# Kernel tuning notes

Hardware: AMD Instinct MI355X
Metric: run time of the kernel (lower is better)

Reference implementation:

```python
import jax, jax.numpy as jnp
import numpy as np

NODE_DIM = 256
EDGE_DIM = 64
TIME_DIM = 1024
HEADS = 8
HEAD_DIM = NODE_DIM // HEADS
MLP = 2
BS, N = 32, 48
BN = BS * N
E = BS * N * (N - 1)


def _lin(k, fin, fout):
    return jax.random.normal(k, (fin, fout), dtype=jnp.float32) / np.sqrt(fin)


def _edge_index():
    idx = np.arange(N)
    src, dst = np.meshgrid(idx, idx, indexing='ij')
    m = src != dst
    src, dst = src[m], dst[m]              # [N*(N-1)] per graph
    offs = (np.arange(BS) * N)[:, None]
    row = (offs + src[None, :]).reshape(-1)
    col = (offs + dst[None, :]).reshape(-1)
    return jnp.asarray(np.stack([row, col]), dtype=jnp.int32)


def setup_inputs() -> dict:
    key = jax.random.key(0)
    ks = jax.random.split(key, 32)
    d = {
        'pos': jax.random.normal(ks[0], (BN, 3), jnp.float32),
        'h': jax.random.normal(ks[1], (BN, NODE_DIM), jnp.float32),
        'edge_attr': jax.random.normal(ks[2], (E, EDGE_DIM), jnp.float32),
        'node_mask': jnp.ones((BN, 1), jnp.float32),
        'node_time_emb': jax.random.normal(ks[3], (BN, TIME_DIM), jnp.float32),
        'edge_time_emb': jax.random.normal(ks[4], (E, TIME_DIM), jnp.float32),
        'edge_index': _edge_index(),
        # edge_emb: Linear(edge_dim+1 -> edge_dim)
        'W_ee': _lin(ks[5], EDGE_DIM + 1, EDGE_DIM), 'b_ee': jnp.zeros((EDGE_DIM,)),
        # AdaLN time MLPs (SiLU -> Linear)
        'W_nt': _lin(ks[6], TIME_DIM, 6 * NODE_DIM), 'b_nt': jnp.zeros((6 * NODE_DIM,)),
        'W_et': _lin(ks[7], TIME_DIM, 6 * EDGE_DIM), 'b_et': jnp.zeros((6 * EDGE_DIM,)),
        # Trans_Layer sparse attention
        'Wq': _lin(ks[8], NODE_DIM, NODE_DIM), 'bq': jnp.zeros((NODE_DIM,)),
        'Wk': _lin(ks[9], NODE_DIM, NODE_DIM), 'bk': jnp.zeros((NODE_DIM,)),
        'Wv': _lin(ks[10], NODE_DIM, NODE_DIM), 'bv': jnp.zeros((NODE_DIM,)),
        'We0': _lin(ks[11], EDGE_DIM, NODE_DIM),
        'We1': _lin(ks[12], EDGE_DIM, NODE_DIM),
        'W_n2e': _lin(ks[13], NODE_DIM, EDGE_DIM), 'b_n2e': jnp.zeros((EDGE_DIM,)),
        # node FFN
        'W_ff1': _lin(ks[14], NODE_DIM, MLP * NODE_DIM), 'b_ff1': jnp.zeros((MLP * NODE_DIM,)),
        'W_ff2': _lin(ks[15], MLP * NODE_DIM, NODE_DIM), 'b_ff2': jnp.zeros((NODE_DIM,)),
        # edge FFN
        'W_ff3': _lin(ks[16], EDGE_DIM, MLP * EDGE_DIM), 'b_ff3': jnp.zeros((MLP * EDGE_DIM,)),
        'W_ff4': _lin(ks[17], MLP * EDGE_DIM, EDGE_DIM), 'b_ff4': jnp.zeros((EDGE_DIM,)),
        # CondEquiUpdate
        'coors_scale': jnp.full((1,), 0.01, jnp.float32),
        'W_ut': _lin(ks[18], TIME_DIM, 2 * NODE_DIM), 'b_ut': jnp.zeros((2 * NODE_DIM,)),
        'W_ui': _lin(ks[19], 2 * NODE_DIM + EDGE_DIM + 1, NODE_DIM), 'b_ui': jnp.zeros((NODE_DIM,)),
        'W_uc1': _lin(ks[20], NODE_DIM, NODE_DIM), 'b_uc1': jnp.zeros((NODE_DIM,)),
        'W_uc2': _lin(ks[21], NODE_DIM, 1),
    }
    return d


def _ln(x):  # LayerNorm, no affine, eps=1e-6
    m = x.mean(-1, keepdims=True)
    v = ((x - m) ** 2).mean(-1, keepdims=True)
    return (x - m) * jax.lax.rsqrt(v + 1e-6)


def _modulate(x, shift, scale):
    return x * (1 + scale) + shift


def _block(pos, h, edge_attr, node_mask, node_time_emb, edge_time_emb, edge_index,
           W_ee, b_ee, W_nt, b_nt, W_et, b_et, Wq, bq, Wk, bk, Wv, bv, We0, We1,
           W_n2e, b_n2e, W_ff1, b_ff1, W_ff2, b_ff2, W_ff3, b_ff3, W_ff4, b_ff4,
           coors_scale, W_ut, b_ut, W_ui, b_ui, W_uc1, b_uc1, W_uc2):
    row, col = edge_index[0], edge_index[1]  # row = source j, col = target i
    diff = pos[row] - pos[col]                              # [E,3]
    dist = jnp.sqrt(jnp.sum(diff * diff, -1, keepdims=True) + 1e-12)  # [E,1]
    ea = jnp.concatenate([dist, edge_attr], -1) @ W_ee + b_ee

    nt = jax.nn.silu(node_time_emb) @ W_nt + b_nt
    n_sh_msa, n_sc_msa, n_g_msa, n_sh_mlp, n_sc_mlp, n_g_mlp = jnp.split(nt, 6, axis=1)
    et = jax.nn.silu(edge_time_emb) @ W_et + b_et
    e_sh_msa, e_sc_msa, e_g_msa, e_sh_mlp, e_sc_mlp, e_g_mlp = jnp.split(et, 6, axis=1)

    hh = _modulate(_ln(h), n_sh_msa, n_sc_msa)
    ea = _modulate(_ln(ea), e_sh_msa, e_sc_msa)

    # sparse multi-head attention over edges (Trans_Layer)
    q = (hh @ Wq + bq).reshape(BN, HEADS, HEAD_DIM)
    k = (hh @ Wk + bk).reshape(BN, HEADS, HEAD_DIM)
    v = (hh @ Wv + bv).reshape(BN, HEADS, HEAD_DIM)
    e0 = (ea @ We0).reshape(E, HEADS, HEAD_DIM)
    e1 = (ea @ We1).reshape(E, HEADS, HEAD_DIM)
    alpha = jnp.sum(q[col] * k[row] * e0, -1) / np.sqrt(HEAD_DIM)  # [E,H]
    mx = jax.ops.segment_max(alpha, col, num_segments=BN)
    ex = jnp.exp(alpha - mx[col])
    den = jax.ops.segment_sum(ex, col, num_segments=BN)
    att = ex / (den[col] + 1e-16)
    msg = v[row] * e1 * att[:, :, None]
    h_node = jax.ops.segment_sum(msg, col, num_segments=BN).reshape(BN, NODE_DIM)

    h_edge = (h_node[row] + h_node[col]) @ W_n2e + b_n2e

    h_node = h + n_g_msa * h_node
    h_node = _modulate(_ln(h_node), n_sh_mlp, n_sc_mlp) * node_mask
    ff = jax.nn.silu(h_node @ W_ff1 + b_ff1) @ W_ff2 + b_ff2
    h_out = (h_node + n_g_mlp * ff) * node_mask

    h_e = edge_attr + e_g_msa * h_edge
    h_e = _modulate(_ln(h_e), e_sh_mlp, e_sc_mlp)
    ffe = jax.nn.silu(h_e @ W_ff3 + b_ff3) @ W_ff4 + b_ff4
    h_edge_out = h_e + e_g_mlp * ffe

    # CondEquiUpdate: equivariant coordinate update
    h_input = jnp.concatenate([h_out[row], h_out[col], h_edge_out, dist], -1)
    nrm = jnp.linalg.norm(diff, axis=-1, keepdims=True)
    cdiff = diff / jnp.clip(nrm, 1e-8) * coors_scale        # CoorsNorm(scale_init=0.01)
    t_shift, t_scale = jnp.split(jax.nn.silu(edge_time_emb) @ W_ut + b_ut, 2, axis=1)
    inv = _modulate(_ln(h_input @ W_ui + b_ui), t_shift, t_scale)
    inv = jnp.tanh(jax.nn.silu(inv @ W_uc1 + b_uc1) @ W_uc2)  # [E,1]
    trans = cdiff * inv
    pos_out = pos + jax.ops.segment_sum(trans, row, num_segments=BN)
    return h_out, h_edge_out, pos_out


def reference(pos, h, edge_attr, node_mask, node_time_emb, edge_time_emb, edge_index,
              W_ee, b_ee, W_nt, b_nt, W_et, b_et, Wq, bq, Wk, bk, Wv, bv, We0, We1,
              W_n2e, b_n2e, W_ff1, b_ff1, W_ff2, b_ff2, W_ff3, b_ff3, W_ff4, b_ff4,
              coors_scale, W_ut, b_ut, W_ui, b_ui, W_uc1, b_uc1, W_uc2):
    return _block(pos, h, edge_attr, node_mask, node_time_emb, edge_time_emb, edge_index,
                  W_ee, b_ee, W_nt, b_nt, W_et, b_et, Wq, bq, Wk, bk, Wv, bv, We0, We1,
                  W_n2e, b_n2e, W_ff1, b_ff1, W_ff2, b_ff2, W_ff3, b_ff3, W_ff4, b_ff4,
                  coors_scale, W_ut, b_ut, W_ui, b_ui, W_uc1, b_uc1, W_uc2)
```

## Files before the change

### kernel.cpp

```cpp
#include <hip/hip_runtime.h>

typedef unsigned short u16;
typedef __attribute__((ext_vector_type(4))) u16 u16x4;
typedef __attribute__((ext_vector_type(8))) u16 u16x8;
typedef __attribute__((ext_vector_type(8))) short s16x8;
typedef __attribute__((ext_vector_type(4))) float f32x4;

#define E_CNT 72192
#define BN_CNT 1536
#define EPG 2256

__device__ __forceinline__ float b2f(u16 u) {
    union { unsigned int i; float f; } x; x.i = ((unsigned int)u) << 16; return x.f;
}
__device__ __forceinline__ u16 f2b(float f) {
    union { float f; unsigned int i; } x; x.f = f;
    unsigned int r = x.i + 0x7fffu + ((x.i >> 16) & 1u);
    return (u16)(r >> 16);
}
__device__ __forceinline__ float siluf(float x) { return x / (1.f + expf(-x)); }

__device__ __forceinline__ void gll16(const void* g, void* l) {
    __builtin_amdgcn_global_load_lds(
        (const __attribute__((address_space(1))) void*)g,
        (__attribute__((address_space(3))) void*)l, 16, 0, 0);
}

__device__ __forceinline__ float wave_ln64(float x) {
    float s = x;
    #pragma unroll
    for (int off = 1; off < 64; off <<= 1) s += __shfl_xor(s, off);
    float mean = s * 0.015625f;
    float d = x - mean;
    float v2 = d * d;
    #pragma unroll
    for (int off = 1; off < 64; off <<= 1) v2 += __shfl_xor(v2, off);
    return d * rsqrtf(v2 * 0.015625f + 1e-6f);
}

__device__ __forceinline__ float block_ln256(float x) {
    __shared__ float tmp[4];
    int t = threadIdx.x;
    float s = x;
    #pragma unroll
    for (int off = 1; off < 64; off <<= 1) s += __shfl_xor(s, off);
    if ((t & 63) == 0) tmp[t >> 6] = s;
    __syncthreads();
    float mean = (tmp[0] + tmp[1] + tmp[2] + tmp[3]) * (1.f / 256.f);
    float d = x - mean;
    float v2 = d * d;
    #pragma unroll
    for (int off = 1; off < 64; off <<= 1) v2 += __shfl_xor(v2, off);
    __syncthreads();
    if ((t & 63) == 0) tmp[t >> 6] = v2;
    __syncthreads();
    float var = (tmp[0] + tmp[1] + tmp[2] + tmp[3]) * (1.f / 256.f);
    return d * rsqrtf(var + 1e-6f);
}

template<int ACT, int OUTBF>
__global__ __launch_bounds__(256) void k_gemm(
    const u16* __restrict__ A, const u16* __restrict__ Bt,
    const float* __restrict__ bias, void* __restrict__ C,
    int M, int N, int K)
{
    __shared__ u16 As[64][40];
    __shared__ u16 Bs[64][40];
    int bn0 = blockIdx.x * 64, bm0 = blockIdx.y * 64;
    int t = threadIdx.x;
    int lane = t & 63, wave = t >> 6;
    int wm = wave >> 1, wn = wave & 1;
    int lr = t >> 2, lc = (t & 3) * 8;
    f32x4 acc[2][2] = {};
    const u16* Ap = A + (size_t)(bm0 + lr) * K + lc;
    const u16* Bp = Bt + (size_t)(bn0 + lr) * K + lc;
    int fr = lane & 15, fk = (lane >> 4) * 8;
    for (int k0 = 0; k0 < K; k0 += 32) {
        *(u16x8*)&As[lr][lc] = *(const u16x8*)(Ap + k0);
        *(u16x8*)&Bs[lr][lc] = *(const u16x8*)(Bp + k0);
        __syncthreads();
        s16x8 a0 = *(const s16x8*)&As[wm * 32 + fr][fk];
        s16x8 a1 = *(const s16x8*)&As[wm * 32 + 16 + fr][fk];
        s16x8 b0 = *(const s16x8*)&Bs[wn * 32 + fr][fk];
        s16x8 b1 = *(const s16x8*)&Bs[wn * 32 + 16 + fr][fk];
        acc[0][0] = __builtin_amdgcn_mfma_f32_16x16x32_bf16(a0, b0, acc[0][0], 0, 0, 0);
        acc[0][1] = __builtin_amdgcn_mfma_f32_16x16x32_bf16(a0, b1, acc[0][1], 0, 0, 0);
        acc[1][0] = __builtin_amdgcn_mfma_f32_16x16x32_bf16(a1, b0, acc[1][0], 0, 0, 0);
        acc[1][1] = __builtin_amdgcn_mfma_f32_16x16x32_bf16(a1, b1, acc[1][1], 0, 0, 0);
        __syncthreads();
    }
    int cIn = lane & 15, r4 = (lane >> 4) * 4;
    #pragma unroll
    for (int i = 0; i < 2; i++)
    #pragma unroll
    for (int j = 0; j < 2; j++) {
        int col = bn0 + wn * 32 + j * 16 + cIn;
        float bv = bias ? bias[col] : 0.f;
        #pragma unroll
        for (int r = 0; r < 4; r++) {
            int rowg = bm0 + wm * 32 + i * 16 + r4 + r;
            float vv = acc[i][j][r] + bv;
            if (ACT == 1) vv = siluf(vv);
            if (OUTBF) ((u16*)C)[(size_t)rowg * N + col] = f2b(vv);
            else       ((float*)C)[(size_t)rowg * N + col] = vv;
        }
    }
}

__global__ __launch_bounds__(256) void k_gemm_ff2ho(
    const u16* __restrict__ A, const u16* __restrict__ Bt,
    const float* __restrict__ bias, const float* __restrict__ hmod,
    const float* __restrict__ nt, const float* __restrict__ mask,
    float* __restrict__ out, u16* __restrict__ hout_bf, int M, int N, int K)
{
    __shared__ u16 As[64][40];
    __shared__ u16 Bs[64][40];
    int bn0 = blockIdx.x * 64, bm0 = blockIdx.y * 64;
    int t = threadIdx.x;
    int lane = t & 63, wave = t >> 6;
    int wm = wave >> 1, wn = wave & 1;
    int lr = t >> 2, lc = (t & 3) * 8;
    f32x4 acc[2][2] = {};
    const u16* Ap = A + (size_t)(bm0 + lr) * K + lc;
    const u16* Bp = Bt + (size_t)(bn0 + lr) * K + lc;
    int fr = lane & 15, fk = (lane >> 4) * 8;
    for (int k0 = 0; k0 < K; k0 += 32) {
        *(u16x8*)&As[lr][lc] = *(const u16x8*)(Ap + k0);
        *(u16x8*)&Bs[lr][lc] = *(const u16x8*)(Bp + k0);
        __syncthreads();
        s16x8 a0 = *(const s16x8*)&As[wm * 32 + fr][fk];
        s16x8 a1 = *(const s16x8*)&As[wm * 32 + 16 + fr][fk];
        s16x8 b0 = *(const s16x8*)&Bs[wn * 32 + fr][fk];
        s16x8 b1 = *(const s16x8*)&Bs[wn * 32 + 16 + fr][fk];
        acc[0][0] = __builtin_amdgcn_mfma_f32_16x16x32_bf16(a0, b0, acc[0][0], 0, 0, 0);
        acc[0][1] = __builtin_amdgcn_mfma_f32_16x16x32_bf16(a0, b1, acc[0][1], 0, 0, 0);
        acc[1][0] = __builtin_amdgcn_mfma_f32_16x16x32_bf16(a1, b0, acc[1][0], 0, 0, 0);
        acc[1][1] = __builtin_amdgcn_mfma_f32_16x16x32_bf16(a1, b1, acc[1][1], 0, 0, 0);
        __syncthreads();
    }
    int cIn = lane & 15, r4 = (lane >> 4) * 4;
    #pragma unroll
    for (int i = 0; i < 2; i++)
    #pragma unroll
    for (int j = 0; j < 2; j++) {
        int col = bn0 + wn * 32 + j * 16 + cIn;
        float bv = bias[col];
        #pragma unroll
        for (int r = 0; r < 4; r++) {
            int rowg = bm0 + wm * 32 + i * 16 + r4 + r;
            float x = acc[i][j][r] + bv;
            float v = (hmod[(size_t)rowg * 256 + col]
                     + nt[(size_t)rowg * 1536 + 1280 + col] * x) * mask[rowg];
            out[(size_t)rowg * 256 + col] = v;
            hout_bf[(size_t)rowg * 256 + col] = f2b(v);
        }
    }
}

__global__ __launch_bounds__(256) void k_gemm_ff4eo(
    const u16* __restrict__ A, const u16* __restrict__ Bt,
    const float* __restrict__ bias, const float* __restrict__ hemod,
    const u16* __restrict__ etf,
    float* __restrict__ out2, u16* __restrict__ heout_bf, int M, int N, int K)
{
    __shared__ u16 As[64][40];
    __shared__ u16 Bs[64][40];
    int bn0 = blockIdx.x * 64, bm0 = blockIdx.y * 64;
    int t = threadIdx.x;
    int lane = t & 63, wave = t >> 6;
    int wm = wave >> 1, wn = wave & 1;
    int lr = t >> 2, lc = (t & 3) * 8;
    f32x4 acc[2][2] = {};
    const u16* Ap = A + (size_t)(bm0 + lr) * K + lc;
    const u16* Bp = Bt + (size_t)(bn0 + lr) * K + lc;
    int fr = lane & 15, fk = (lane >> 4) * 8;
    for (int k0 = 0; k0 < K; k0 += 32) {
        *(u16x8*)&As[lr][lc] = *(const u16x8*)(Ap + k0);
        *(u16x8*)&Bs[lr][lc] = *(const u16x8*)(Bp + k0);
        __syncthreads();
        s16x8 a0 = *(const s16x8*)&As[wm * 32 + fr][fk];
        s16x8 a1 = *(const s16x8*)&As[wm * 32 + 16 + fr][fk];
        s16x8 b0 = *(const s16x8*)&Bs[wn * 32 + fr][fk];
        s16x8 b1 = *(const s16x8*)&Bs[wn * 32 + 16 + fr][fk];
        acc[0][0] = __builtin_amdgcn_mfma_f32_16x16x32_bf16(a0, b0, acc[0][0], 0, 0, 0);
        acc[0][1] = __builtin_amdgcn_mfma_f32_16x16x32_bf16(a0, b1, acc[0][1], 0, 0, 0);
        acc[1][0] = __builtin_amdgcn_mfma_f32_16x16x32_bf16(a1, b0, acc[1][0], 0, 0, 0);
        acc[1][1] = __builtin_amdgcn_mfma_f32_16x16x32_bf16(a1, b1, acc[1][1], 0, 0, 0);
        __syncthreads();
    }
    int cIn = lane & 15, r4 = (lane >> 4) * 4;
    #pragma unroll
    for (int i = 0; i < 2; i++)
    #pragma unroll
    for (int j = 0; j < 2; j++) {
        int col = bn0 + wn * 32 + j * 16 + cIn;
        float bv = bias[col];
        #pragma unroll
        for (int r = 0; r < 4; r++) {
            int rowg = bm0 + wm * 32 + i * 16 + r4 + r;
            float x = acc[i][j][r] + bv;
            float v = hemod[(size_t)rowg * 64 + col]
                    + b2f(etf[(size_t)rowg * 896 + 320 + col]) * x;
            out2[(size_t)rowg * 64 + col] = v;
            heout_bf[(size_t)rowg * 64 + col] = f2b(v);
        }
    }
}

template<int ACT, int OUTBF>
__global__ __launch_bounds__(256) void k_gemm128(
    const u16* __restrict__ A, const u16* __restrict__ Bt,
    const float* __restrict__ bias, void* __restrict__ C,
    int M, int N, int K)
{
    __shared__ u16 As[3][128 * 32];
    __shared__ u16 Bs[3][128 * 32];
    const int t = threadIdx.x;
    const int lane = t & 63, wv = t >> 6;
    const int wm = wv >> 1, wn = wv & 1;
    const int nwg = gridDim.x * gridDim.y;
    const int orig = blockIdx.y * gridDim.x + blockIdx.x;
    const int q8 = nwg >> 3, r8 = nwg & 7;
    const int xcd = orig & 7, lin = orig >> 3;
    const int wgid = (xcd < r8 ? xcd * (q8 + 1) : r8 * (q8 + 1) + (xcd - r8) * q8) + lin;
    const int bxs = wgid % gridDim.x, bys = wgid / gridDim.x;
    const int bn0 = bxs * 128, bm0 = bys * 128;
    const int srow = t >> 2;
    const int scol = ((t & 3) ^ ((t >> 3) & 3)) * 8;
    const u16* Ap = A + (size_t)(bm0 + srow) * K + scol;
    const u16* Bp = Bt + (size_t)(bn0 + srow) * K + scol;
    const size_t rstep = (size_t)64 * K;
    const int woff = wv * 16 * 32;
    const int fr = lane & 15;
    const int fkc = (((lane >> 4) ^ ((fr >> 1) & 3)) * 8);
    f32x4 acc[4][4] = {};
    const int NT = K >> 5;

    auto STAGE = [&](int b, int ko) {
        gll16(Ap + ko, &As[b][woff]);
        gll16(Ap + ko + rstep, &As[b][woff + 64 * 32]);
        gll16(Bp + ko, &Bs[b][woff]);
        gll16(Bp + ko + rstep, &Bs[b][woff + 64 * 32]);
    };
    auto COMPUTE = [&](int b) {
        const u16* aBase = &As[b][wm * 64 * 32];
        const u16* bBase = &Bs[b][wn * 64 * 32];
        s16x8 af[4], bfr[4];
        #pragma unroll
        for (int m = 0; m < 4; m++) af[m] = *(const s16x8*)&aBase[(m * 16 + fr) * 32 + fkc];
        #pragma unroll
        for (int n = 0; n < 4; n++) bfr[n] = *(const s16x8*)&bBase[(n * 16 + fr) * 32 + fkc];
        #pragma unroll
        for (int m = 0; m < 4; m++)
        #pragma unroll
        for (int n = 0; n < 4; n++)
            acc[m][n] = __builtin_amdgcn_mfma_f32_16x16x32_bf16(af[m], bfr[n], acc[m][n], 0, 0, 0);
    };

    STAGE(0, 0);
    if (NT > 1) STAGE(1, 32);
    int cur = 0;
    for (int tt = 0; tt < NT; tt++) {
        if (tt + 2 < NT) STAGE((cur + 2) % 3, (tt + 2) * 32);
        __builtin_amdgcn_sched_barrier(0);
        int ahead = NT - 1 - tt; if (ahead > 2) ahead = 2;
        if (ahead == 2)      asm volatile("s_waitcnt vmcnt(8)" ::: "memory");
        else if (ahead == 1) asm volatile("s_waitcnt vmcnt(4)" ::: "memory");
        else                 asm volatile("s_waitcnt vmcnt(0)" ::: "memory");
        __builtin_amdgcn_sched_barrier(0);
        __builtin_amdgcn_s_barrier();
        COMPUTE(cur);
        __builtin_amdgcn_s_barrier();
        __builtin_amdgcn_sched_barrier(0);
        cur = (cur + 1) % 3;
    }

    const int cIn = lane & 15, r4 = (lane >> 4) * 4;
    #pragma unroll
    for (int n = 0; n < 4; n++) {
        int col = bn0 + wn * 64 + n * 16 + cIn;
        float bv = bias ? bias[col] : 0.f;
        #pragma unroll
        for (int m = 0; m < 4; m++) {
            #pragma unroll
            for (int r = 0; r < 4; r++) {
                int rowg = bm0 + wm * 64 + m * 16 + r4 + r;
                float vv = acc[m][n][r] + bv;
                if (ACT == 1) vv = siluf(vv);
                if (OUTBF) ((u16*)C)[(size_t)rowg * N + col] = f2b(vv);
                else       ((float*)C)[(size_t)rowg * N + col] = vv;
            }
        }
    }
}

struct GJob {
    const u16* A; const u16* Bt; const float* bias; void* C;
    int M, N, K, gx, nwg, act, outbf;
};

__global__ __launch_bounds__(256) void k_gemm128_dual(GJob ja, GJob jb)
{
    const bool first = (int)blockIdx.x < ja.nwg;
    const GJob J = first ? ja : jb;
    const int orig = first ? blockIdx.x : blockIdx.x - ja.nwg;
    __shared__ u16 As[3][128 * 32];
    __shared__ u16 Bs[3][128 * 32];
    const int t = threadIdx.x;
    const int lane = t & 63, wv = t >> 6;
    const int wm = wv >> 1, wn = wv & 1;
    const int K = J.K;
    const int q8 = J.nwg >> 3, r8 = J.nwg & 7;
    const int xcd = orig & 7, lin = orig >> 3;
    const int wgid = (xcd < r8 ? xcd * (q8 + 1) : r8 * (q8 + 1) + (xcd - r8) * q8) + lin;
    const int bxs = wgid % J.gx, bys = wgid / J.gx;
    const int bn0 = bxs * 128, bm0 = bys * 128;
    const int srow = t >> 2;
    const int scol = ((t & 3) ^ ((t >> 3) & 3)) * 8;
    const u16* Ap = J.A + (size_t)(bm0 + srow) * K + scol;
    const u16* Bp = J.Bt + (size_t)(bn0 + srow) * K + scol;
    const size_t rstep = (size_t)64 * K;
    const int woff = wv * 16 * 32;
    const int fr = lane & 15;
    const int fkc = (((lane >> 4) ^ ((fr >> 1) & 3)) * 8);
    f32x4 acc[4][4] = {};
    const int NT = K >> 5;

    auto STAGE = [&](int b, int ko) {
        gll16(Ap + ko, &As[b][woff]);
        gll16(Ap + ko + rstep, &As[b][woff + 64 * 32]);
        gll16(Bp + ko, &Bs[b][woff]);
        gll16(Bp + ko + rstep, &Bs[b][woff + 64 * 32]);
    };
    auto COMPUTE = [&](int b) {
        const u16* aBase = &As[b][wm * 64 * 32];
        const u16* bBase = &Bs[b][wn * 64 * 32];
        s16x8 af[4], bfr[4];
        #pragma unroll
        for (int m = 0; m < 4; m++) af[m] = *(const s16x8*)&aBase[(m * 16 + fr) * 32 + fkc];
        #pragma unroll
        for (int n = 0; n < 4; n++) bfr[n] = *(const s16x8*)&bBase[(n * 16 + fr) * 32 + fkc];
        #pragma unroll
        for (int m = 0; m < 4; m++)
        #pragma unroll
        for (int n = 0; n < 4; n++)
            acc[m][n] = __builtin_amdgcn_mfma_f32_16x16x32_bf16(af[m], bfr[n], acc[m][n], 0, 0, 0);
    };

    STAGE(0, 0);
    if (NT > 1) STAGE(1, 32);
    int cur = 0;
    for (int tt = 0; tt < NT; tt++) {
        if (tt + 2 < NT) STAGE((cur + 2) % 3, (tt + 2) * 32);
        __builtin_amdgcn_sched_barrier(0);
        int ahead = NT - 1 - tt; if (ahead > 2) ahead = 2;
        if (ahead == 2)      asm volatile("s_waitcnt vmcnt(8)" ::: "memory");
        else if (ahead == 1) asm volatile("s_waitcnt vmcnt(4)" ::: "memory");
        else                 asm volatile("s_waitcnt vmcnt(0)" ::: "memory");
        __builtin_amdgcn_sched_barrier(0);
        __builtin_amdgcn_s_barrier();
        COMPUTE(cur);
        __builtin_amdgcn_s_barrier();
        __builtin_amdgcn_sched_barrier(0);
        cur = (cur + 1) % 3;
    }

    const int cIn = lane & 15, r4 = (lane >> 4) * 4;
    #pragma unroll
    for (int n = 0; n < 4; n++) {
        int col = bn0 + wn * 64 + n * 16 + cIn;
        float bv = J.bias ? J.bias[col] : 0.f;
        #pragma unroll
        for (int m = 0; m < 4; m++) {
            #pragma unroll
            for (int r = 0; r < 4; r++) {
                int rowg = bm0 + wm * 64 + m * 16 + r4 + r;
                float vv = acc[m][n][r] + bv;
                if (J.act) vv = siluf(vv);
                if (J.outbf) ((u16*)J.C)[(size_t)rowg * J.N + col] = f2b(vv);
                else         ((float*)J.C)[(size_t)rowg * J.N + col] = vv;
            }
        }
    }
}

struct ConvJob { const float* W; u16* Wt; int ldw, k0, n0, K, tile_start, tiles_k; };
struct CopyJob { const float* src; float* dst; int n; };
struct BatchArgs {
    ConvJob cj[17]; CopyJob cp[5]; int conv_blocks;
    const float* sA; u16* sOA; int n4A;
    const float* sB; u16* sOB; int n4B; int silu_blocks;
};

__global__ __launch_bounds__(256) void k_prep(BatchArgs a)
{
    __shared__ float ls[64][65];
    int b = blockIdx.x;
    int t = threadIdx.x;
    if (b < a.conv_blocks) {
        int j = 0;
        #pragma unroll 1
        while (j + 1 < 17 && a.cj[j + 1].tile_start <= b) ++j;
        const ConvJob J = a.cj[j];
        int local = b - J.tile_start;
        int tk = local % J.tiles_k, tn = local / J.tiles_k;
        int k0 = tk * 64, n0 = tn * 64;
        int cn = t & 63, rk = t >> 6;
        #pragma unroll
        for (int p = 0; p < 16; p++) {
            int kk = p * 4 + rk;
            ls[kk][cn] = J.W[(size_t)(J.k0 + k0 + kk) * J.ldw + J.n0 + n0 + cn];
        }
        __syncthreads();
        int ck = t & 63, rn = t >> 6;
        #pragma unroll
        for (int p = 0; p < 16; p++) {
            int nn = p * 4 + rn;
            J.Wt[(size_t)(n0 + nn) * J.K + k0 + ck] = f2b(ls[ck][nn]);
        }
    } else if (b < a.conv_blocks + 5) {
        int c = b - a.conv_blocks;
        const CopyJob C = a.cp[c];
        for (int i = t; i < C.n; i += 256) C.dst[i] = C.src[i];
    } else {
        int sb = b - a.conv_blocks - 5;
        int total = a.n4A + a.n4B;
        int stride = a.silu_blocks * 256;
        for (int i = sb * 256 + t; i < total; i += stride) {
            const float* in; u16* out; int idx;
            if (i < a.n4A) { in = a.sA; out = a.sOA; idx = i; }
            else           { in = a.sB; out = a.sOB; idx = i - a.n4A; }
            f32x4 v = *(const f32x4*)(in + (size_t)idx * 4);
            u16x4 o;
            #pragma unroll
            for (int j = 0; j < 4; j++) o[j] = f2b(siluf(v[j]));
            *(u16x4*)(out + (size_t)idx * 4) = o;
        }
    }
}

__global__ __launch_bounds__(256) void k_edge_pre(
    const float* __restrict__ pos, const float* __restrict__ edge_attr,
    const int* __restrict__ ei, const float* __restrict__ W_ee,
    const float* __restrict__ b_ee, const float* __restrict__ coors_scale,
    const u16* __restrict__ etf,
    u16* __restrict__ ea_mod, float* __restrict__ dist, float* __restrict__ cdiff)
{
    __shared__ float Ws[65][64];
    int t = threadIdx.x;
    for (int i = t; i < 65 * 64; i += 256) Ws[i >> 6][i & 63] = W_ee[i];
    __syncthreads();
    int l = t & 63;
    float bee = b_ee[l];
    float cscale = coors_scale[0];
    for (int g = 0; g < 16; g++) {
        int e = blockIdx.x * 64 + g * 4 + (t >> 6);
        int row = ei[e], col = ei[E_CNT + e];
        float d0 = pos[row * 3 + 0] - pos[col * 3 + 0];
        float d1 = pos[row * 3 + 1] - pos[col * 3 + 1];
        float d2 = pos[row * 3 + 2] - pos[col * 3 + 2];
        float ssq = d0 * d0 + d1 * d1 + d2 * d2;
        float dst = sqrtf(ssq + 1e-12f);
        float nrm = sqrtf(ssq);
        float cs = cscale / fmaxf(nrm, 1e-8f);
        if (l == 0) {
            dist[e] = dst;
            cdiff[e * 3 + 0] = d0 * cs; cdiff[e * 3 + 1] = d1 * cs; cdiff[e * 3 + 2] = d2 * cs;
        }
        float attr = edge_attr[(size_t)e * 64 + l];
        float acc = dst * Ws[0][l];
        for (int f = 0; f < 64; f++) acc += __shfl(attr, f) * Ws[1 + f][l];
        acc += bee;
        float y = wave_ln64(acc);
        const u16* ep = etf + (size_t)e * 896;
        float m = y * (1.f + b2f(ep[64 + l])) + b2f(ep[l]);
        ea_mod[(size_t)e * 64 + l] = f2b(m);
    }
}

__global__ __launch_bounds__(256) void k_node_hh(
    const float* __restrict__ h, const float* __restrict__ nt, u16* __restrict__ hh)
{
    int n = blockIdx.x, c = threadIdx.x;
    float x = h[(size_t)n * 256 + c];
    float y = block_ln256(x);
    float m = y * (1.f + nt[(size_t)n * 1536 + 256 + c]) + nt[(size_t)n * 1536 + c];
    hh[(size_t)n * 256 + c] = f2b(m);
}

__global__ __launch_bounds__(256) void k_agg(
    const float* __restrict__ qkv, const u16* __restrict__ e01,
    float* __restrict__ hnode, u16* __restrict__ hnode_bf)
{
    int n = blockIdx.x;
    int b = n / 48, i = n % 48;
    int t = threadIdx.x;
    __shared__ float qs[8][33];
    __shared__ float att[47][8];
    __shared__ float mxs[8], dens[8];
    __shared__ int elist[47], slist[47];
    qs[t >> 5][t & 31] = qkv[(size_t)n * 768 + t];
    if (t < 47) {
        int s = t + (t >= i ? 1 : 0);
        slist[t] = s;
        elist[t] = b * EPG + s * 47 + (i < s ? i : i - 1);
    }
    __syncthreads();
    for (int idx = t; idx < 376; idx += 256) {
        int j = idx >> 3, hh = idx & 7;
        int src = b * 48 + slist[j];
        int e = elist[j];
        const float* kp = qkv + (size_t)src * 768 + 256 + hh * 32;
        const u16* ep = e01 + (size_t)e * 512 + hh * 32;
        float p = 0.f;
        #pragma unroll
        for (int d = 0; d < 32; d++) p += qs[hh][d] * kp[d] * b2f(ep[d]);
        att[j][hh] = p * 0.17677669529663687f;
    }
    __syncthreads();
    if (t < 8) {
        float m = -1e30f;
        for (int j = 0; j < 47; j++) m = fmaxf(m, att[j][t]);
        float den = 0.f;
        for (int j = 0; j < 47; j++) den += expf(att[j][t] - m);
        mxs[t] = m; dens[t] = den + 1e-16f;
    }
    __syncthreads();
    for (int idx = t; idx < 376; idx += 256) {
        int j = idx >> 3, hh = idx & 7;
        att[j][hh] = expf(att[j][hh] - mxs[hh]) / dens[hh];
    }
    __syncthreads();
    int c = t, hh = t >> 5;
    float acc = 0.f;
    for (int j = 0; j < 47; j++) {
        int src = b * 48 + slist[j];
        int e = elist[j];
        acc += att[j][hh] * qkv[(size_t)src * 768 + 512 + c] * b2f(e01[(size_t)e * 512 + 256 + c]);
    }
    hnode[(size_t)n * 256 + c] = acc;
    hnode_bf[(size_t)n * 256 + c] = f2b(acc);
}

__global__ __launch_bounds__(256) void k_mods(
    const float* __restrict__ h, const float* __restrict__ hnode_raw,
    const float* __restrict__ nt, const float* __restrict__ mask,
    float* __restrict__ hmod, u16* __restrict__ hmod_bf,
    const float* __restrict__ Q1, const float* __restrict__ b_n2e,
    const float* __restrict__ edge_attr, const int* __restrict__ ei,
    const u16* __restrict__ etf, float* __restrict__ hemod, u16* __restrict__ hemod_bf)
{
    if ((int)blockIdx.x < BN_CNT) {
        int n = blockIdx.x, c = threadIdx.x;
        float x = h[(size_t)n * 256 + c] + nt[(size_t)n * 1536 + 512 + c] * hnode_raw[(size_t)n * 256 + c];
        float y = block_ln256(x);
        float m = (y * (1.f + nt[(size_t)n * 1536 + 1024 + c]) + nt[(size_t)n * 1536 + 768 + c]) * mask[n];
        hmod[(size_t)n * 256 + c] = m;
        hmod_bf[(size_t)n * 256 + c] = f2b(m);
    } else {
        int bb = blockIdx.x - BN_CNT;
        int l = threadIdx.x & 63;
        float bn2e = b_n2e[l];
        for (int g = 0; g < 4; g++) {
            int e = bb * 16 + g * 4 + (threadIdx.x >> 6);
            int row = ei[e], col = ei[E_CNT + e];
            float hedge = Q1[(size_t)row * 64 + l] + Q1[(size_t)col * 64 + l] + bn2e;
            const u16* ep = etf + (size_t)e * 896;
            float x = edge_attr[(size_t)e * 64 + l] + b2f(ep[128 + l]) * hedge;
            float y = wave_ln64(x);
            float m = y * (1.f + b2f(ep[256 + l])) + b2f(ep[192 + l]);
            hemod[(size_t)e * 64 + l] = m;
            hemod_bf[(size_t)e * 64 + l] = f2b(m);
        }
    }
}

__global__ __launch_bounds__(256) void k_inv_pre4(
    const float* __restrict__ p12,
    const u16* __restrict__ P3, const float* __restrict__ dist,
    const float* __restrict__ W_ui, const float* __restrict__ b_ui,
    const int* __restrict__ ei, const u16* __restrict__ etf, u16* __restrict__ invmod)
{
    int e = blockIdx.x * 4 + (threadIdx.x >> 6);
    int l = threadIdx.x & 63;
    int c = l * 4;
    int row = ei[e], col = ei[E_CNT + e];
    f32x4 pa = *(const f32x4*)(p12 + (size_t)row * 512 + c);
    f32x4 pb = *(const f32x4*)(p12 + (size_t)col * 512 + 256 + c);
    u16x4 p3 = *(const u16x4*)(P3 + (size_t)e * 256 + c);
    f32x4 wui = *(const f32x4*)(W_ui + 576 * 256 + c);
    f32x4 bui = *(const f32x4*)(b_ui + c);
    float dd = dist[e];
    float x[4];
    float s = 0.f;
    #pragma unroll
    for (int j = 0; j < 4; j++) {
        x[j] = pa[j] + pb[j] + b2f(p3[j]) + dd * wui[j] + bui[j];
        s += x[j];
    }
    #pragma unroll
    for (int off = 1; off < 64; off <<= 1) s += __shfl_xor(s, off);
    float mean = s * (1.f / 256.f);
    float v2 = 0.f;
    #pragma unroll
    for (int j = 0; j < 4; j++) {
        float d = x[j] - mean;
        v2 += d * d;
    }
    #pragma unroll
    for (int off = 1; off < 64; off <<= 1) v2 += __shfl_xor(v2, off);
    float rs = rsqrtf(v2 * (1.f / 256.f) + 1e-6f);
    const u16* ep = etf + (size_t)e * 896;
    u16x4 sc = *(const u16x4*)(ep + 640 + c);
    u16x4 sh = *(const u16x4*)(ep + 384 + c);
    u16x4 o;
    #pragma unroll
    for (int j = 0; j < 4; j++) {
        float y = (x[j] - mean) * rs;
        o[j] = f2b(y * (1.f + b2f(sc[j])) + b2f(sh[j]));
    }
    *(u16x4*)(invmod + (size_t)e * 256 + c) = o;
}

__global__ __launch_bounds__(256) void k_inv(const u16* __restrict__ uc1,
                                             const float* __restrict__ W_uc2,
                                             float* __restrict__ inv)
{
    int l = threadIdx.x & 63;
    const float* w = W_uc2 + l * 4;
    float w0 = w[0], w1 = w[1], w2 = w[2], w3 = w[3];
    for (int g = 0; g < 4; g++) {
        int e = blockIdx.x * 16 + g * 4 + (threadIdx.x >> 6);
        u16x4 v = *(const u16x4*)(uc1 + (size_t)e * 256 + l * 4);
        float s = b2f(v[0]) * w0 + b2f(v[1]) * w1 + b2f(v[2]) * w2 + b2f(v[3]) * w3;
        #pragma unroll
        for (int off = 1; off < 64; off <<= 1) s += __shfl_xor(s, off);
        if (l == 0) inv[e] = tanhf(s);
    }
}

__global__ void k_pos(const float* __restrict__ pos, const float* __restrict__ cdiff,
                      const float* __restrict__ inv, float* __restrict__ out3)
{
    int n = blockIdx.x * 256 + threadIdx.x;
    if (n >= BN_CNT) return;
    int b = n / 48, s = n % 48;
    int e0 = b * EPG + s * 47;
    float a0 = 0.f, a1 = 0.f, a2 = 0.f;
    for (int j = 0; j < 47; j++) {
        float f = inv[e0 + j];
        a0 += cdiff[(size_t)(e0 + j) * 3 + 0] * f;
        a1 += cdiff[(size_t)(e0 + j) * 3 + 1] * f;
        a2 += cdiff[(size_t)(e0 + j) * 3 + 2] * f;
    }
    out3[n * 3 + 0] = pos[n * 3 + 0] + a0;
    out3[n * 3 + 1] = pos[n * 3 + 1] + a1;
    out3[n * 3 + 2] = pos[n * 3 + 2] + a2;
}

extern "C" void kernel_launch(void* const* d_in, const int* in_sizes, int n_in,
                              void* d_out, int out_size, void* d_ws, size_t ws_size,
                              hipStream_t stream)
{
    (void)in_sizes; (void)n_in; (void)out_size; (void)ws_size;
    const float* pos       = (const float*)d_in[0];
    const float* h         = (const float*)d_in[1];
    const float* edge_attr = (const float*)d_in[2];
    const float* node_mask = (const float*)d_in[3];
    const float* nte       = (const float*)d_in[4];
    const float* ete       = (const float*)d_in[5];
    const int*   ei        = (const int*)d_in[6];
    const float* W_ee = (const float*)d_in[7];  const float* b_ee = (const float*)d_in[8];
    const float* W_nt = (const float*)d_in[9];  const float* b_nt = (const float*)d_in[10];
    const float* W_et = (const float*)d_in[11]; const float* b_et = (const float*)d_in[12];
    const float* Wq  = (const float*)d_in[13];  const float* bq  = (const float*)d_in[14];
    const float* Wk  = (const float*)d_in[15];  const float* bk  = (const float*)d_in[16];
    const float* Wv  = (const float*)d_in[17];  const float* bv  = (const float*)d_in[18];
    const float* We0 = (const float*)d_in[19];  const float* We1 = (const float*)d_in[20];
    const float* W_n2e = (const float*)d_in[21]; const float* b_n2e = (const float*)d_in[22];
    const float* W_ff1 = (const float*)d_in[23]; const float* b_ff1 = (const float*)d_in[24];
    const float* W_ff2 = (const float*)d_in[25]; const float* b_ff2 = (const float*)d_in[26];
    const float* W_ff3 = (const float*)d_in[27]; const float* b_ff3 = (const float*)d_in[28];
    const float* W_ff4 = (const float*)d_in[29]; const float* b_ff4 = (const float*)d_in[30];
    const float* coors_scale = (const float*)d_in[31];
    const float* W_ut = (const float*)d_in[32]; const float* b_ut = (const float*)d_in[33];
    const float* W_ui = (const float*)d_in[34]; const float* b_ui = (const float*)d_in[35];
    const float* W_uc1 = (const float*)d_in[36]; const float* b_uc1 = (const float*)d_in[37];
    const float* W_uc2 = (const float*)d_in[38];

    const size_t E = E_CNT;
    char* ws = (char*)d_ws;
    size_t off = 0;
    auto AL = [&](size_t b) { size_t o = off; off += (b + 255) & ~(size_t)255; return o; };

    size_t o_wtcat  = AL(896 * 1024 * 2);
    size_t o_wtnt   = AL(1536 * 1024 * 2);
    size_t o_wtqkv  = AL(768 * 256 * 2);
    size_t o_wte01  = AL(512 * 64 * 2);
    size_t o_wtn2e  = AL(64 * 256 * 2);
    size_t o_wtff1  = AL(512 * 256 * 2), o_wtff2 = AL(256 * 512 * 2);
    size_t o_wtff3  = AL(128 * 64 * 2),  o_wtff4 = AL(64 * 128 * 2);
    size_t o_wtuiab = AL(512 * 256 * 2);
    size_t o_wtuic  = AL(256 * 64 * 2),  o_wtuc1 = AL(256 * 256 * 2);
    size_t o_bias896 = AL(896 * 4);
    size_t o_bias768 = AL(768 * 4);
    size_t o_reg1 = AL(E * 1024 * 2);
    size_t o_etf  = AL(E * 896 * 2);
    size_t o_ntes = AL(1536 * 1024 * 2);
    size_t o_ntf  = AL((size_t)1536 * 1536 * 4);
    size_t o_eamod = AL(E * 64 * 2);
    size_t o_dist = AL(E * 4), o_cdiff = AL(E * 12);
    size_t o_qkv  = AL(1536 * 768 * 4);
    size_t o_reg3 = AL(E * 512 * 2);
    size_t o_hnode = AL(1536 * 256 * 4), o_hnodebf = AL(1536 * 256 * 2);
    size_t o_q1 = AL(1536 * 64 * 4);
    size_t o_hh = AL(1536 * 256 * 2);
    size_t o_hmod = AL(1536 * 256 * 4), o_hmodbf = AL(1536 * 256 * 2);
    size_t o_ff1 = AL(1536 * 512 * 2);
    size_t o_houtbf = AL(1536 * 256 * 2);
    size_t o_hemod = AL(E * 64 * 4), o_hemodbf = AL(E * 64 * 2);
    size_t o_p12 = AL(1536 * 512 * 4);
    size_t o_inv = AL(E * 4);
    size_t o_etes = o_reg1;
    size_t o_p3 = o_reg1;
    size_t o_invmod = o_reg1 + E * 256 * 2;
    size_t o_uc1o = o_reg1 + E * 256 * 4;
    size_t o_e01 = o_reg3;
    size_t o_ffem = o_reg3;
    size_t o_heoutbf = o_reg3 + E * 128 * 2 + E * 64 * 4;

    #define WSU(o) ((u16*)(ws + (o)))
    #define WSF(o) ((float*)(ws + (o)))

    {
        BatchArgs a;
        int s = 0; int j = 0;
        auto add = [&](const float* W, u16* Wt, int ldw, int k0, int n0, int K, int NC) {
            a.cj[j++] = ConvJob{W, Wt, ldw, k0, n0, K, s, K / 64};
            s += (K / 64) * (NC / 64);
        };
        add(W_et, WSU(o_wtcat), 384, 0, 0, 1024, 384);
        add(W_ut, WSU(o_wtcat) + (size_t)384 * 1024, 512, 0, 0, 1024, 512);
        add(W_nt, WSU(o_wtnt), 1536, 0, 0, 1024, 1536);
        add(Wq, WSU(o_wtqkv), 256, 0, 0, 256, 256);
        add(Wk, WSU(o_wtqkv) + (size_t)256 * 256, 256, 0, 0, 256, 256);
        add(Wv, WSU(o_wtqkv) + (size_t)512 * 256, 256, 0, 0, 256, 256);
        add(We0, WSU(o_wte01), 256, 0, 0, 64, 256);
        add(We1, WSU(o_wte01) + (size_t)256 * 64, 256, 0, 0, 64, 256);
        add(W_n2e, WSU(o_wtn2e), 64, 0, 0, 256, 64);
        add(W_ff1, WSU(o_wtff1), 512, 0, 0, 256, 512);
        add(W_ff2, WSU(o_wtff2), 256, 0, 0, 512, 256);
        add(W_ff3, WSU(o_wtff3), 128, 0, 0, 64, 128);
        add(W_ff4, WSU(o_wtff4), 64, 0, 0, 128, 64);
        add(W_ui, WSU(o_wtuiab), 256, 0, 0, 256, 256);
        add(W_ui, WSU(o_wtuiab) + (size_t)256 * 256, 256, 256, 0, 256, 256);
        add(W_ui, WSU(o_wtuic), 256, 512, 0, 64, 256);
        add(W_uc1, WSU(o_wtuc1), 256, 0, 0, 256, 256);
        a.conv_blocks = s;
        a.cp[0] = CopyJob{b_et, WSF(o_bias896), 384};
        a.cp[1] = CopyJob{b_ut, WSF(o_bias896) + 384, 512};
        a.cp[2] = CopyJob{bq, WSF(o_bias768), 256};
        a.cp[3] = CopyJob{bk, WSF(o_bias768) + 256, 256};
        a.cp[4] = CopyJob{bv, WSF(o_bias768) + 512, 256};
        a.sA = ete; a.sOA = WSU(o_etes); a.n4A = (int)(E * 1024 / 4);
        a.sB = nte; a.sOB = WSU(o_ntes); a.n4B = 1536 * 1024 / 4;
        a.silu_blocks = 2048;
        k_prep<<<s + 5 + 2048, 256, 0, stream>>>(a);
    }

    {
        GJob ja{WSU(o_etes), WSU(o_wtcat), WSF(o_bias896), WSU(o_etf),
                E_CNT, 896, 1024, 7, 3948, 0, 1};
        GJob jb{WSU(o_ntes), WSU(o_wtnt), b_nt, WSF(o_ntf),
                1536, 1536, 1024, 12, 144, 0, 0};
        k_gemm128_dual<<<3948 + 144, 256, 0, stream>>>(ja, jb);
    }

    k_edge_pre<<<1128, 256, 0, stream>>>(pos, edge_attr, ei, W_ee, b_ee, coors_scale,
                                         WSU(o_etf), WSU(o_eamod), WSF(o_dist), WSF(o_cdiff));
    k_node_hh<<<1536, 256, 0, stream>>>(h, WSF(o_ntf), WSU(o_hh));

    {
        GJob ja{WSU(o_eamod), WSU(o_wte01), nullptr, WSU(o_e01),
                E_CNT, 512, 64, 4, 2256, 0, 1};
        GJob jb{WSU(o_hh), WSU(o_wtqkv), WSF(o_bias768), WSF(o_qkv),
                1536, 768, 256, 6, 72, 0, 0};
        k_gemm128_dual<<<2256 + 72, 256, 0, stream>>>(ja, jb);
    }
    k_agg<<<1536, 256, 0, stream>>>(WSF(o_qkv), WSU(o_e01), WSF(o_hnode), WSU(o_hnodebf));

    k_gemm<0, 0><<<dim3(1, 24), 256, 0, stream>>>(WSU(o_hnodebf), WSU(o_wtn2e), nullptr, WSF(o_q1), 1536, 64, 256);

    k_mods<<<BN_CNT + 4512, 256, 0, stream>>>(
        h, WSF(o_hnode), WSF(o_ntf), node_mask, WSF(o_hmod), WSU(o_hmodbf),
        WSF(o_q1), b_n2e, edge_attr, ei, WSU(o_etf), WSF(o_hemod), WSU(o_hemodbf));

    {
        GJob ja{WSU(o_hemodbf), WSU(o_wtff3), b_ff3, WSU(o_ffem),
                E_CNT, 128, 64, 1, 564, 1, 1};
        GJob jb{WSU(o_hmodbf), WSU(o_wtff1), b_ff1, WSU(o_ff1),
                1536, 512, 256, 4, 48, 1, 1};
        k_gemm128_dual<<<564 + 48, 256, 0, stream>>>(ja, jb);
    }

    k_gemm_ff2ho<<<dim3(4, 24), 256, 0, stream>>>(WSU(o_ff1), WSU(o_wtff2), b_ff2,
                                                  WSF(o_hmod), WSF(o_ntf), node_mask,
                                                  (float*)d_out, WSU(o_houtbf), 1536, 256, 512);
    k_gemm_ff4eo<<<dim3(1, 1128), 256, 0, stream>>>(WSU(o_ffem), WSU(o_wtff4), b_ff4,
                                                    WSF(o_hemod), WSU(o_etf),
                                                    (float*)d_out + 393216, WSU(o_heoutbf), E_CNT, 64, 128);

    {
        GJob ja{WSU(o_heoutbf), WSU(o_wtuic), nullptr, WSU(o_p3),
                E_CNT, 256, 64, 2, 1128, 0, 1};
        GJob jb{WSU(o_houtbf), WSU(o_wtuiab), nullptr, WSF(o_p12),
                1536, 512, 256, 4, 48, 0, 0};
        k_gemm128_dual<<<1128 + 48, 256, 0, stream>>>(ja, jb);
    }
    k_inv_pre4<<<18048, 256, 0, stream>>>(WSF(o_p12), WSU(o_p3), WSF(o_dist),
                                          W_ui, b_ui, ei, WSU(o_etf), WSU(o_invmod));
    k_gemm128<1, 1><<<dim3(2, 564), 256, 0, stream>>>(WSU(o_invmod), WSU(o_wtuc1), b_uc1, WSU(o_uc1o), E_CNT, 256, 256);
    k_inv<<<4512, 256, 0, stream>>>(WSU(o_uc1o), W_uc2, WSF(o_inv));
    k_pos<<<6, 256, 0, stream>>>(pos, WSF(o_cdiff), WSF(o_inv), (float*)d_out + 393216 + E_CNT * 64);

    #undef WSU
    #undef WSF
}
```

Before: 675.2 us.

## Merge independent kernels into combined launches and fuse n2e projection into aggregation

Combines the edge-pre and node-LN kernels into one launch with block-range dispatch, and merges the two FF-output GEMM epilogue kernels into one launch the same way. It also folds the small hnode×W_n2e GEMM into the attention aggregation kernel, which now computes q1 per node with a shared-memory dot product. This removes three kernel launches and their serialization gaps. The cost is a scalar per-block reduction in place of a small MFMA GEMM, plus extra shared memory in k_agg.

```diff
diff --git a/kernel.cpp b/kernel.cpp
--- a/kernel.cpp
+++ b/kernel.cpp
@@ -107,15 +107,27 @@
     }
 }
 
-__global__ __launch_bounds__(256) void k_gemm_ff2ho(
-    const u16* __restrict__ A, const u16* __restrict__ Bt,
-    const float* __restrict__ bias, const float* __restrict__ hmod,
+__global__ __launch_bounds__(256) void k_ffout(
+    const u16* __restrict__ A1, const u16* __restrict__ Bt1,
+    const float* __restrict__ bias1, const float* __restrict__ hmod,
     const float* __restrict__ nt, const float* __restrict__ mask,
-    float* __restrict__ out, u16* __restrict__ hout_bf, int M, int N, int K)
+    float* __restrict__ out1, u16* __restrict__ hout_bf,
+    const u16* __restrict__ A2, const u16* __restrict__ Bt2,
+    const float* __restrict__ bias2, const float* __restrict__ hemod,
+    const u16* __restrict__ etf,
+    float* __restrict__ out2, u16* __restrict__ heout_bf)
 {
     __shared__ u16 As[64][40];
     __shared__ u16 Bs[64][40];
-    int bn0 = blockIdx.x * 64, bm0 = blockIdx.y * 64;
+    const bool first = (int)blockIdx.x < 96;
+    const u16* A = first ? A1 : A2;
+    const u16* Bt = first ? Bt1 : Bt2;
+    const float* bias = first ? bias1 : bias2;
+    const int N = first ? 256 : 64;
+    const int K = first ? 512 : 128;
+    int bn0, bm0;
+    if (first) { bn0 = ((int)blockIdx.x % 4) * 64; bm0 = ((int)blockIdx.x / 4) * 64; }
+    else       { bn0 = 0; bm0 = ((int)blockIdx.x - 96) * 64; }
     int t = threadIdx.x;
     int lane = t & 63, wave = t >> 6;
     int wm = wave >> 1, wn = wave & 1;
@@ -149,60 +161,17 @@
         for (int r = 0; r < 4; r++) {
             int rowg = bm0 + wm * 32 + i * 16 + r4 + r;
             float x = acc[i][j][r] + bv;
-            float v = (hmod[(size_t)rowg * 256 + col]
-                     + nt[(size_t)rowg * 1536 + 1280 + col] * x) * mask[rowg];
-            out[(size_t)rowg * 256 + col] = v;
-            hout_bf[(size_t)rowg * 256 + col] = f2b(v);
-        }
-    }
-}
-
-__global__ __launch_bounds__(256) void k_gemm_ff4eo(
-    const u16* __restrict__ A, const u16* __restrict__ Bt,
-    const float* __restrict__ bias, const float* __restrict__ hemod,
-    const u16* __restrict__ etf,
-    float* __restrict__ out2, u16* __restrict__ heout_bf, int M, int N, int K)
-{
-    __shared__ u16 As[64][40];
-    __shared__ u16 Bs[64][40];
-    int bn0 = blockIdx.x * 64, bm0 = blockIdx.y * 64;
-    int t = threadIdx.x;
-    int lane = t & 63, wave = t >> 6;
-    int wm = wave >> 1, wn = wave & 1;
-    int lr = t >> 2, lc = (t & 3) * 8;
-    f32x4 acc[2][2] = {};
-    const u16* Ap = A + (size_t)(bm0 + lr) * K + lc;
-    const u16* Bp = Bt + (size_t)(bn0 + lr) * K + lc;
-    int fr = lane & 15, fk = (lane >> 4) * 8;
-    for (int k0 = 0; k0 < K; k0 += 32) {
-        *(u16x8*)&As[lr][lc] = *(const u16x8*)(Ap + k0);
-        *(u16x8*)&Bs[lr][lc] = *(const u16x8*)(Bp + k0);
-        __syncthreads();
-        s16x8 a0 = *(const s16x8*)&As[wm * 32 + fr][fk];
-        s16x8 a1 = *(const s16x8*)&As[wm * 32 + 16 + fr][fk];
-        s16x8 b0 = *(const s16x8*)&Bs[wn * 32 + fr][fk];
-        s16x8 b1 = *(const s16x8*)&Bs[wn * 32 + 16 + fr][fk];
-        acc[0][0] = __builtin_amdgcn_mfma_f32_16x16x32_bf16(a0, b0, acc[0][0], 0, 0, 0);
-        acc[0][1] = __builtin_amdgcn_mfma_f32_16x16x32_bf16(a0, b1, acc[0][1], 0, 0, 0);
-        acc[1][0] = __builtin_amdgcn_mfma_f32_16x16x32_bf16(a1, b0, acc[1][0], 0, 0, 0);
-        acc[1][1] = __builtin_amdgcn_mfma_f32_16x16x32_bf16(a1, b1, acc[1][1], 0, 0, 0);
-        __syncthreads();
-    }
-    int cIn = lane & 15, r4 = (lane >> 4) * 4;
-    #pragma unroll
-    for (int i = 0; i < 2; i++)
-    #pragma unroll
-    for (int j = 0; j < 2; j++) {
-        int col = bn0 + wn * 32 + j * 16 + cIn;
-        float bv = bias[col];
-        #pragma unroll
-        for (int r = 0; r < 4; r++) {
-            int rowg = bm0 + wm * 32 + i * 16 + r4 + r;
-            float x = acc[i][j][r] + bv;
-            float v = hemod[(size_t)rowg * 64 + col]
-                    + b2f(etf[(size_t)rowg * 896 + 320 + col]) * x;
-            out2[(size_t)rowg * 64 + col] = v;
-            heout_bf[(size_t)rowg * 64 + col] = f2b(v);
+            if (first) {
+                float v = (hmod[(size_t)rowg * 256 + col]
+                         + nt[(size_t)rowg * 1536 + 1280 + col] * x) * mask[rowg];
+                out1[(size_t)rowg * 256 + col] = v;
+                hout_bf[(size_t)rowg * 256 + col] = f2b(v);
+            } else {
+                float v = hemod[(size_t)rowg * 64 + col]
+                        + b2f(etf[(size_t)rowg * 896 + 320 + col]) * x;
+                out2[(size_t)rowg * 64 + col] = v;
+                heout_bf[(size_t)rowg * 64 + col] = f2b(v);
+            }
         }
     }
 }
@@ -439,58 +408,58 @@
     }
 }
 
-__global__ __launch_bounds__(256) void k_edge_pre(
+__global__ __launch_bounds__(256) void k_pre2(
     const float* __restrict__ pos, const float* __restrict__ edge_attr,
     const int* __restrict__ ei, const float* __restrict__ W_ee,
     const float* __restrict__ b_ee, const float* __restrict__ coors_scale,
     const u16* __restrict__ etf,
-    u16* __restrict__ ea_mod, float* __restrict__ dist, float* __restrict__ cdiff)
-{
-    __shared__ float Ws[65][64];
+    u16* __restrict__ ea_mod, float* __restrict__ dist, float* __restrict__ cdiff,
+    const float* __restrict__ h, const float* __restrict__ nt, u16* __restrict__ hh)
+{
     int t = threadIdx.x;
-    for (int i = t; i < 65 * 64; i += 256) Ws[i >> 6][i & 63] = W_ee[i];
-    __syncthreads();
-    int l = t & 63;
-    float bee = b_ee[l];
-    float cscale = coors_scale[0];
-    for (int g = 0; g < 16; g++) {
-        int e = blockIdx.x * 64 + g * 4 + (t >> 6);
-        int row = ei[e], col = ei[E_CNT + e];
-        float d0 = pos[row * 3 + 0] - pos[col * 3 + 0];
-        float d1 = pos[row * 3 + 1] - pos[col * 3 + 1];
-        float d2 = pos[row * 3 + 2] - pos[col * 3 + 2];
-        float ssq = d0 * d0 + d1 * d1 + d2 * d2;
-        float dst = sqrtf(ssq + 1e-12f);
-        float nrm = sqrtf(ssq);
-        float cs = cscale / fmaxf(nrm, 1e-8f);
-        if (l == 0) {
-            dist[e] = dst;
-            cdiff[e * 3 + 0] = d0 * cs; cdiff[e * 3 + 1] = d1 * cs; cdiff[e * 3 + 2] = d2 * cs;
+    if ((int)blockIdx.x < 1128) {
+        __shared__ float Ws[65][64];
+        for (int i = t; i < 65 * 64; i += 256) Ws[i >> 6][i & 63] = W_ee[i];
+        __syncthreads();
+        int l = t & 63;
+        float bee = b_ee[l];
+        float cscale = coors_scale[0];
+        for (int g = 0; g < 16; g++) {
+            int e = blockIdx.x * 64 + g * 4 + (t >> 6);
+            int row = ei[e], col = ei[E_CNT + e];
+            float d0 = pos[row * 3 + 0] - pos[col * 3 + 0];
+            float d1 = pos[row * 3 + 1] - pos[col * 3 + 1];
+            float d2 = pos[row * 3 + 2] - pos[col * 3 + 2];
+            float ssq = d0 * d0 + d1 * d1 + d2 * d2;
+            float dst = sqrtf(ssq + 1e-12f);
+            float nrm = sqrtf(ssq);
+            float cs = cscale / fmaxf(nrm, 1e-8f);
+            if (l == 0) {
+                dist[e] = dst;
+                cdiff[e * 3 + 0] = d0 * cs; cdiff[e * 3 + 1] = d1 * cs; cdiff[e * 3 + 2] = d2 * cs;
+            }
+            float attr = edge_attr[(size_t)e * 64 + l];
+            float acc = dst * Ws[0][l];
+            for (int f = 0; f < 64; f++) acc += __shfl(attr, f) * Ws[1 + f][l];
+            acc += bee;
+            float y = wave_ln64(acc);
+            const u16* ep = etf + (size_t)e * 896;
+            float m = y * (1.f + b2f(ep[64 + l])) + b2f(ep[l]);
+            ea_mod[(size_t)e * 64 + l] = f2b(m);
         }
-        float attr = edge_attr[(size_t)e * 64 + l];
-        float acc = dst * Ws[0][l];
-        for (int f = 0; f < 64; f++) acc += __shfl(attr, f) * Ws[1 + f][l];
-        acc += bee;
-        float y = wave_ln64(acc);
-        const u16* ep = etf + (size_t)e * 896;
-        float m = y * (1.f + b2f(ep[64 + l])) + b2f(ep[l]);
-        ea_mod[(size_t)e * 64 + l] = f2b(m);
-    }
-}
-
-__global__ __launch_bounds__(256) void k_node_hh(
-    const float* __restrict__ h, const float* __restrict__ nt, u16* __restrict__ hh)
-{
-    int n = blockIdx.x, c = threadIdx.x;
-    float x = h[(size_t)n * 256 + c];
-    float y = block_ln256(x);
-    float m = y * (1.f + nt[(size_t)n * 1536 + 256 + c]) + nt[(size_t)n * 1536 + c];
-    hh[(size_t)n * 256 + c] = f2b(m);
+    } else {
+        int n = blockIdx.x - 1128, c = t;
+        float x = h[(size_t)n * 256 + c];
+        float y = block_ln256(x);
+        float m = y * (1.f + nt[(size_t)n * 1536 + 256 + c]) + nt[(size_t)n * 1536 + c];
+        hh[(size_t)n * 256 + c] = f2b(m);
+    }
 }
 
 __global__ __launch_bounds__(256) void k_agg(
     const float* __restrict__ qkv, const u16* __restrict__ e01,
-    float* __restrict__ hnode, u16* __restrict__ hnode_bf)
+    const u16* __restrict__ wtn2e,
+    float* __restrict__ hnode, u16* __restrict__ hnode_bf, float* __restrict__ q1)
 {
     int n = blockIdx.x;
     int b = n / 48, i = n % 48;
@@ -499,6 +468,8 @@
     __shared__ float att[47][8];
     __shared__ float mxs[8], dens[8];
     __shared__ int elist[47], slist[47];
+    __shared__ float hs[256];
+    __shared__ float q1s[4][64];
     qs[t >> 5][t & 31] = qkv[(size_t)n * 768 + t];
     if (t < 47) {
         int s = t + (t >= i ? 1 : 0);
@@ -538,8 +509,20 @@
         int e = elist[j];
         acc += att[j][hh] * qkv[(size_t)src * 768 + 512 + c] * b2f(e01[(size_t)e * 512 + 256 + c]);
     }
+    u16 abf = f2b(acc);
     hnode[(size_t)n * 256 + c] = acc;
-    hnode_bf[(size_t)n * 256 + c] = f2b(acc);
+    hnode_bf[(size_t)n * 256 + c] = abf;
+    hs[c] = b2f(abf);
+    __syncthreads();
+    int jq = t & 63, p = t >> 6;
+    const u16* wrow = wtn2e + (size_t)jq * 256 + p * 64;
+    const float* hrow = hs + p * 64;
+    float part = 0.f;
+    #pragma unroll
+    for (int cc = 0; cc < 64; cc++) part += hrow[cc] * b2f(wrow[cc]);
+    q1s[p][jq] = part;
+    __syncthreads();
+    if (t < 64) q1[(size_t)n * 64 + t] = q1s[0][t] + q1s[1][t] + q1s[2][t] + q1s[3][t];
 }
 
 __global__ __launch_bounds__(256) void k_mods(
@@ -776,9 +759,10 @@
         k_gemm128_dual<<<3948 + 144, 256, 0, stream>>>(ja, jb);
     }
 
-    k_edge_pre<<<1128, 256, 0, stream>>>(pos, edge_attr, ei, W_ee, b_ee, coors_scale,
-                                         WSU(o_etf), WSU(o_eamod), WSF(o_dist), WSF(o_cdiff));
-    k_node_hh<<<1536, 256, 0, stream>>>(h, WSF(o_ntf), WSU(o_hh));
+    k_pre2<<<1128 + 1536, 256, 0, stream>>>(
+        pos, edge_attr, ei, W_ee, b_ee, coors_scale,
+        WSU(o_etf), WSU(o_eamod), WSF(o_dist), WSF(o_cdiff),
+        h, WSF(o_ntf), WSU(o_hh));
 
     {
         GJob ja{WSU(o_eamod), WSU(o_wte01), nullptr, WSU(o_e01),
@@ -787,9 +771,8 @@
                 1536, 768, 256, 6, 72, 0, 0};
         k_gemm128_dual<<<2256 + 72, 256, 0, stream>>>(ja, jb);
     }
-    k_agg<<<1536, 256, 0, stream>>>(WSF(o_qkv), WSU(o_e01), WSF(o_hnode), WSU(o_hnodebf));
-
-    k_gemm<0, 0><<<dim3(1, 24), 256, 0, stream>>>(WSU(o_hnodebf), WSU(o_wtn2e), nullptr, WSF(o_q1), 1536, 64, 256);
+    k_agg<<<1536, 256, 0, stream>>>(WSF(o_qkv), WSU(o_e01), WSU(o_wtn2e),
+                                    WSF(o_hnode), WSU(o_hnodebf), WSF(o_q1));
 
     k_mods<<<BN_CNT + 4512, 256, 0, stream>>>(
         h, WSF(o_hnode), WSF(o_ntf), node_mask, WSF(o_hmod), WSU(o_hmodbf),
@@ -803,12 +786,11 @@
         k_gemm128_dual<<<564 + 48, 256, 0, stream>>>(ja, jb);
     }
 
-    k_gemm_ff2ho<<<dim3(4, 24), 256, 0, stream>>>(WSU(o_ff1), WSU(o_wtff2), b_ff2,
-                                                  WSF(o_hmod), WSF(o_ntf), node_mask,
-                                                  (float*)d_out, WSU(o_houtbf), 1536, 256, 512);
-    k_gemm_ff4eo<<<dim3(1, 1128), 256, 0, stream>>>(WSU(o_ffem), WSU(o_wtff4), b_ff4,
-                                                    WSF(o_hemod), WSU(o_etf),
-                                                    (float*)d_out + 393216, WSU(o_heoutbf), E_CNT, 64, 128);
+    k_ffout<<<96 + 1128, 256, 0, stream>>>(
+        WSU(o_ff1), WSU(o_wtff2), b_ff2, WSF(o_hmod), WSF(o_ntf), node_mask,
+        (float*)d_out, WSU(o_houtbf),
+        WSU(o_ffem), WSU(o_wtff4), b_ff4, WSF(o_hemod), WSU(o_etf),
+        (float*)d_out + 393216, WSU(o_heoutbf));
 
     {
         GJob ja{WSU(o_heoutbf), WSU(o_wtuic), nullptr, WSU(o_p3),
```

Result: no change. 678.0 us (+0.4%).
